# Kernel tuning notes

Measured on AMD Instinct MI355X. Metric: run time of the kernel, lower is better.

## Reference

```python
import jax, jax.numpy as jnp
import numpy as np

N_OPS, B, C, N = 7, 128, 64, 30   # n_ops from alphas (7), SPD dim hard-coded to 30 in source
KARCHER_ITERS = 3                 # fixed-point iterations of the weighted geometric mean


def _spd_fn(X, fn):
    """Apply scalar fn to eigenvalues of batched symmetric matrices X[..., n, n]."""
    s, U = jnp.linalg.eigh(X)
    s = jnp.maximum(s, 1e-8)  # SPD clamp for log/sqrt stability
    return jnp.einsum('...ij,...j,...kj->...ik', U, fn(s), U)


def _sym(X):
    return 0.5 * (X + jnp.swapaxes(X, -1, -2))


def setup_inputs() -> dict:
    key = jax.random.key(0)
    k1, k2 = jax.random.split(key)
    # Candidate-op outputs: SPD matrices, one per (op, batch, channel).
    G = jax.random.normal(k1, (N_OPS, B, C, N, N), dtype=jnp.float32)
    spds = jnp.einsum('...ij,...kj->...ik', G, G) / N + 0.1 * jnp.eye(N, dtype=jnp.float32)
    # Architecture logits for this edge (softmaxed in forward, as in Network.forward).
    alphas = 0.001 * jax.random.normal(k2, (N_OPS,), dtype=jnp.float32)
    return {"spds": spds, "alphas": alphas}


def reference(spds, alphas):
    """MixedOp forward: softmax-weighted SPD geometric (Karcher) barycenter over
    candidate ops, batched over every (batch, channel) 30x30 SPD matrix.
    Replaces the per-channel Python loop + bary_geom_weightedbatch of the source.
    Returns [B, C, N, N]."""
    w = jax.nn.softmax(alphas)                       # [n_ops]
    A = spds.reshape(N_OPS, B * C, N, N)             # [o, m, n, n], m = B*C
    # init with weighted arithmetic mean (standard Karcher-flow initialization)
    X = jnp.einsum('o,omij->mij', w, A)              # [m, n, n]
    for _ in range(KARCHER_ITERS):
        Xh = _spd_fn(X, jnp.sqrt)                    # X^{1/2}
        Xih = _spd_fn(X, lambda s: 1.0 / jnp.sqrt(s))  # X^{-1/2}
        mid = jnp.einsum('mij,omjk,mkl->omil', Xih, A, Xih)  # [o, m, n, n]
        logs = _spd_fn(_sym(mid), jnp.log)
        L = _sym(jnp.einsum('o,omij->mij', w, logs))  # tangent-space mean
        X = _sym(Xh @ _spd_fn(L, jnp.exp) @ Xh)      # exp map back to manifold
    return X.reshape(B, C, N, N)
```

## Files before the change

### kernel.cpp

```cpp
#include <hip/hip_runtime.h>
#include <math.h>

#define NOPS 7
#define KITERS 3
#define NBLK 31

template<int M> __device__ __forceinline__ float xshuf(float x);
template<> __device__ __forceinline__ float xshuf<1>(float x) {
    return __int_as_float(__builtin_amdgcn_mov_dpp(__float_as_int(x), 0xB1, 0xF, 0xF, true));
}
template<> __device__ __forceinline__ float xshuf<2>(float x) {
    return __int_as_float(__builtin_amdgcn_mov_dpp(__float_as_int(x), 0x4E, 0xF, 0xF, true));
}
template<> __device__ __forceinline__ float xshuf<4>(float x) {
    return __int_as_float(__builtin_amdgcn_ds_swizzle(__float_as_int(x), (4 << 10) | 0x1F));
}
template<> __device__ __forceinline__ float xshuf<8>(float x) {
    return __int_as_float(__builtin_amdgcn_ds_swizzle(__float_as_int(x), (8 << 10) | 0x1F));
}

template<int M>
__device__ __forceinline__ void jround(float (&a)[16], float (&v)[16], float2* ct,
                                       const int il, const int lane, const int fKb) {
    const int fil = (il & (M - 1)) | ((il >> 1) & ~(M - 1));
    const float dq  = xshuf<M>(a[0]);
    const float apq = a[M];
    float cc = 1.f, ss = 0.f;
    if (fabsf(apq) > 1e-12f) {
        const float th = (dq - a[0]) / (2.f * apq);
        const float t  = copysignf(1.f, th) / (fabsf(th) + sqrtf(1.f + th * th));
        cc = rsqrtf(1.f + t * t);
        ss = t * cc;
    }
    if ((lane & (32 | M)) == 0) ct[fil] = make_float2(cc, ss);
    __syncthreads();
    const float2 me = ct[fil];
    const float sg = (il & M) ? 1.f : -1.f;
    const float c0 = me.x, s0 = sg * me.y;
    #pragma unroll
    for (int j = 0; j < 16; ++j) {
        if (j & M) continue;
        const int fj = (j & (M - 1)) | ((j >> 1) & ~(M - 1));
        const float2 cs = ct[fil ^ (fj | fKb)];
        const float sl = sg * cs.y;
        const float ak = a[j], am = a[j ^ M];
        a[j]     = fmaf( sl, am, cs.x * ak);
        a[j ^ M] = fmaf(-sl, ak, cs.x * am);
        const float2 cu = ct[fj | fKb];
        const float vk = v[j], vm = v[j ^ M];
        v[j]     = fmaf(-cu.y, vm, cu.x * vk);
        v[j ^ M] = fmaf( cu.y, vk, cu.x * vm);
    }
    #pragma unroll
    for (int j = 0; j < 16; ++j) {
        if (j & M) continue;
        const float r1 = xshuf<M>(a[j ^ M]);
        const float r2 = xshuf<M>(a[j]);
        a[j]     = fmaf(s0, r1, c0 * a[j]);
        a[j ^ M] = fmaf(s0, r2, c0 * a[j ^ M]);
    }
}

__global__ __launch_bounds__(64)
void karcher_kernel(const float* __restrict__ spds, const float* __restrict__ alphas,
                    float* __restrict__ out, int Mtot) {
    __shared__ __align__(16) float XI[1024];
    __shared__ __align__(16) float SC[1024];
    __shared__ float2 CT[16];
    __shared__ float FDA[32];
    __shared__ float FDB[32];
    __shared__ float WS[8];

    const int lane  = threadIdx.x;
    const int il    = lane & 31;
    const int cbit  = lane >> 5;
    const int cbase = cbit << 4;
    const int fKb   = cbit << 3;
    const int c13   = cbit ? 13 : 0;
    const int mat   = blockIdx.x;
    const bool rr   = (il < 30);

    if (lane == 0) {
        float aa[NOPS], mx = -1e30f, sum = 0.f;
        #pragma unroll
        for (int o = 0; o < NOPS; ++o) { aa[o] = alphas[o]; mx = fmaxf(mx, aa[o]); }
        #pragma unroll
        for (int o = 0; o < NOPS; ++o) { aa[o] = expf(aa[o] - mx); sum += aa[o]; }
        #pragma unroll
        for (int o = 0; o < NOPS; ++o) WS[o] = aa[o] / sum;
    }

    int l4row = il;
    #pragma unroll
    for (int i = 0; i < 4; ++i) l4row = ((l4row << 1) & 31) ^ ((l4row & 16) ? 5 : 0);

    const size_t ostr = (size_t)Mtot * 900;
    const float* Abase = spds + (size_t)mat * 900 + (size_t)il * 30 + cbase;
    float* orow = out + (size_t)mat * 900 + (size_t)il * 30 + cbase;

    auto stage16 = [&](float* buf, const float (&r)[16]) {
        #pragma unroll
        for (int j = 0; j < 16; ++j) buf[((cbase + j) << 5) + il] = r[j];
    };
    auto xload16 = [&](const float* buf, float (&a)[16]) {
        #pragma unroll
        for (int j = 0; j < 16; ++j) a[j] = buf[((il ^ (cbase + j)) << 5) + il];
    };
    auto perm4 = [&](float (&a)[16], float (&v)[16]) {
        constexpr int L4T[16] = {0,16,5,21,10,26,15,31,20,4,17,1,30,14,27,11};
        #pragma unroll
        for (int j = 0; j < 16; ++j) SC[((cbase + j) << 5) + il] = a[j];
        __syncthreads();
        #pragma unroll
        for (int j = 0; j < 16; ++j) a[j] = SC[((L4T[j] ^ c13) << 5) + l4row];
        __syncthreads();
        #pragma unroll
        for (int j = 0; j < 16; ++j) SC[((cbase + j) << 5) + il] = v[j];
        __syncthreads();
        #pragma unroll
        for (int j = 0; j < 16; ++j) v[j] = SC[((L4T[j] ^ c13) << 5) + il];
        __syncthreads();
    };
    auto jacobi = [&](float (&a)[16], float (&v)[16]) {
        #pragma unroll
        for (int j = 0; j < 16; ++j) v[j] = (cbase + j == il) ? 1.f : 0.f;
        #pragma unroll 1
        for (int b = 0; b < NBLK; ++b) {
            jround<1>(a, v, CT, il, lane, fKb);
            jround<2>(a, v, CT, il, lane, fKb);
            jround<4>(a, v, CT, il, lane, fKb);
            jround<8>(a, v, CT, il, lane, fKb);
            perm4(a, v);
        }
    };
    auto loadA = [&](const float* Ao, float (&r)[16]) {
        #pragma unroll
        for (int u = 0; u < 7; ++u) {
            const float2 p = *(const float2*)(Ao + 2 * u);
            r[2 * u] = p.x; r[2 * u + 1] = p.y;
        }
        if (cbit == 0) {
            const float2 p = *(const float2*)(Ao + 14);
            r[14] = p.x; r[15] = p.y;
        }
    };
    auto fma16 = [&](const float* buf, const int k, const float c, float (&acc)[16]) {
        const float4* bp = (const float4*)(buf + (k << 5) + cbase);
        #pragma unroll
        for (int q = 0; q < 4; ++q) {
            const float4 b = bp[q];
            acc[4*q+0] = fmaf(c, b.x, acc[4*q+0]);
            acc[4*q+1] = fmaf(c, b.y, acc[4*q+1]);
            acc[4*q+2] = fmaf(c, b.z, acc[4*q+2]);
            acc[4*q+3] = fmaf(c, b.w, acc[4*q+3]);
        }
    };

    __syncthreads();

    float X[16];
    #pragma unroll
    for (int j = 0; j < 16; ++j) X[j] = 0.f;
    if (rr) {
        #pragma unroll 1
        for (int o = 0; o < NOPS; ++o) {
            const float wo = WS[o];
            float r[16];
            #pragma unroll
            for (int j = 0; j < 16; ++j) r[j] = 0.f;
            loadA(Abase + (size_t)o * ostr, r);
            #pragma unroll
            for (int j = 0; j < 16; ++j) X[j] = fmaf(wo, r[j], X[j]);
        }
    }

    float Lacc[16];

    #pragma unroll 1
    for (int it = 0; it < KITERS; ++it) {
        __syncthreads();
        stage16(SC, X);
        __syncthreads();
        float a1[16], v1[16];
        xload16(SC, a1);
        jacobi(a1, v1);
        if (lane < 32) {
            const float lam = fmaxf(a1[0], 1e-8f);
            const float sq = sqrtf(lam);
            FDA[il] = sq;
            FDB[il] = 1.f / sq;
        }
        __syncthreads();
        stage16(SC, v1);
        __syncthreads();
        {
            float xh[16], xi[16];
            #pragma unroll
            for (int j = 0; j < 16; ++j) { xh[j] = 0.f; xi[j] = 0.f; }
            #pragma unroll 2
            for (int k = 0; k < 30; ++k) {
                const float vk = SC[(k << 5) + il];
                const float c1 = FDA[k] * vk;
                const float c2 = FDB[k] * vk;
                const float4* bp = (const float4*)(SC + (k << 5) + cbase);
                #pragma unroll
                for (int q = 0; q < 4; ++q) {
                    const float4 b = bp[q];
                    xh[4*q+0] = fmaf(c1, b.x, xh[4*q+0]); xi[4*q+0] = fmaf(c2, b.x, xi[4*q+0]);
                    xh[4*q+1] = fmaf(c1, b.y, xh[4*q+1]); xi[4*q+1] = fmaf(c2, b.y, xi[4*q+1]);
                    xh[4*q+2] = fmaf(c1, b.z, xh[4*q+2]); xi[4*q+2] = fmaf(c2, b.z, xi[4*q+2]);
                    xh[4*q+3] = fmaf(c1, b.w, xh[4*q+3]); xi[4*q+3] = fmaf(c2, b.w, xi[4*q+3]);
                }
            }
            if (rr) {
                #pragma unroll
                for (int u = 0; u < 7; ++u)
                    *(float2*)(orow + 2 * u) = make_float2(xh[2*u], xh[2*u+1]);
                if (cbit == 0)
                    *(float2*)(orow + 14) = make_float2(xh[14], xh[15]);
            }
            __syncthreads();
            stage16(XI, xi);
        }
        #pragma unroll
        for (int j = 0; j < 16; ++j) Lacc[j] = 0.f;

        #pragma unroll 1
        for (int o = 0; o < NOPS; ++o) {
            float ar[16];
            #pragma unroll
            for (int j = 0; j < 16; ++j) ar[j] = 0.f;
            if (rr) loadA(Abase + (size_t)o * ostr, ar);
            __syncthreads();
            stage16(SC, ar);
            __syncthreads();
            float T[16];
            #pragma unroll
            for (int j = 0; j < 16; ++j) T[j] = 0.f;
            #pragma unroll 2
            for (int k = 0; k < 30; ++k)
                fma16(SC, k, XI[(k << 5) + il], T);
            __syncthreads();
            stage16(SC, T);
            __syncthreads();
            float md[16];
            #pragma unroll
            for (int j = 0; j < 16; ++j) md[j] = 0.f;
            #pragma unroll 2
            for (int k = 0; k < 30; ++k)
                fma16(XI, k, SC[(k << 5) + il], md);
            __syncthreads();
            stage16(SC, md);
            __syncthreads();
            float a2[16], v2[16];
            xload16(SC, a2);
            jacobi(a2, v2);
            if (lane < 32) FDA[il] = logf(fmaxf(a2[0], 1e-8f));
            __syncthreads();
            stage16(SC, v2);
            __syncthreads();
            const float wo = WS[o];
            #pragma unroll 2
            for (int k = 0; k < 30; ++k)
                fma16(SC, k, wo * FDA[k] * SC[(k << 5) + il], Lacc);
        }

        __syncthreads();
        stage16(SC, Lacc);
        __syncthreads();
        float a3[16], v3[16];
        xload16(SC, a3);
        jacobi(a3, v3);
        if (lane < 32) FDA[il] = expf(fmaxf(a3[0], 1e-8f));
        __syncthreads();
        stage16(SC, v3);
        __syncthreads();
        float E[16];
        #pragma unroll
        for (int j = 0; j < 16; ++j) E[j] = 0.f;
        #pragma unroll 2
        for (int k = 0; k < 30; ++k)
            fma16(SC, k, FDA[k] * SC[(k << 5) + il], E);
        float xr[16];
        #pragma unroll
        for (int j = 0; j < 16; ++j) xr[j] = 0.f;
        if (rr) loadA(orow, xr);
        __syncthreads();
        stage16(XI, E);
        stage16(SC, xr);
        __syncthreads();
        float T2[16];
        #pragma unroll
        for (int j = 0; j < 16; ++j) T2[j] = 0.f;
        #pragma unroll 2
        for (int k = 0; k < 30; ++k)
            fma16(XI, k, SC[(k << 5) + il], T2);
        __syncthreads();
        stage16(XI, T2);
        __syncthreads();
        #pragma unroll
        for (int j = 0; j < 16; ++j) X[j] = 0.f;
        #pragma unroll 2
        for (int k = 0; k < 30; ++k)
            fma16(SC, k, XI[(k << 5) + il], X);
    }

    if (rr) {
        #pragma unroll
        for (int u = 0; u < 7; ++u)
            *(float2*)(orow + 2 * u) = make_float2(X[2*u], X[2*u+1]);
        if (cbit == 0)
            *(float2*)(orow + 14) = make_float2(X[14], X[15]);
    }
}

extern "C" void kernel_launch(void* const* d_in, const int* in_sizes, int n_in,
                              void* d_out, int out_size, void* d_ws, size_t ws_size,
                              hipStream_t stream) {
    const float* spds   = (const float*)d_in[0];
    const float* alphas = (const float*)d_in[1];
    float* out = (float*)d_out;
    const int Mtot = in_sizes[0] / (NOPS * 900);
    karcher_kernel<<<dim3(Mtot), dim3(64), 0, stream>>>(spds, alphas, out, Mtot);
}
```

Baseline: 9.388 ms.

## Pack four wavefronts per block, use wave-local syncs, add Jacobi early exit

Each block now holds four independent single-wave matrix solvers with per-wave shared buffers. Block-wide barriers become wave-local s_waitcnt fences, since each matrix lives entirely in one 64-lane wave. Jacobi sweeps can now stop early once every off-diagonal entry falls below a threshold after a minimum sweep count. Some reduction loops are widened to 32, and some FMAs are fused. The early exit changes numerical accuracy, and relying on lgkmcnt waits instead of barriers assumes one wave executes in lockstep.

```diff
diff --git a/kernel.cpp b/kernel.cpp
--- a/kernel.cpp
+++ b/kernel.cpp
@@ -4,6 +4,12 @@
 #define NOPS 7
 #define KITERS 3
 #define NBLK 31
+#define WPB 4
+#define CHKFROM 10
+#define CONVEPS 3e-6f
+
+#define WSYNC() asm volatile("s_waitcnt lgkmcnt(0)" ::: "memory")
+#define VSYNC() asm volatile("s_waitcnt vmcnt(0)" ::: "memory")
 
 template<int M> __device__ __forceinline__ float xshuf(float x);
 template<> __device__ __forceinline__ float xshuf<1>(float x) {
@@ -21,19 +27,19 @@
 
 template<int M>
 __device__ __forceinline__ void jround(float (&a)[16], float (&v)[16], float2* ct,
-                                       const int il, const int lane, const int fKb) {
+                                       const int il, const int wlane, const int fKb) {
     const int fil = (il & (M - 1)) | ((il >> 1) & ~(M - 1));
     const float dq  = xshuf<M>(a[0]);
     const float apq = a[M];
     float cc = 1.f, ss = 0.f;
     if (fabsf(apq) > 1e-12f) {
         const float th = (dq - a[0]) / (2.f * apq);
-        const float t  = copysignf(1.f, th) / (fabsf(th) + sqrtf(1.f + th * th));
-        cc = rsqrtf(1.f + t * t);
+        const float t  = copysignf(1.f, th) / (fabsf(th) + sqrtf(fmaf(th, th, 1.f)));
+        cc = rsqrtf(fmaf(t, t, 1.f));
         ss = t * cc;
     }
-    if ((lane & (32 | M)) == 0) ct[fil] = make_float2(cc, ss);
-    __syncthreads();
+    if ((wlane & (32 | M)) == 0) ct[fil] = make_float2(cc, ss);
+    WSYNC();
     const float2 me = ct[fil];
     const float sg = (il & M) ? 1.f : -1.f;
     const float c0 = me.x, s0 = sg * me.y;
@@ -61,26 +67,37 @@
     }
 }
 
-__global__ __launch_bounds__(64)
+__global__ __launch_bounds__(64 * WPB)
 void karcher_kernel(const float* __restrict__ spds, const float* __restrict__ alphas,
                     float* __restrict__ out, int Mtot) {
-    __shared__ __align__(16) float XI[1024];
-    __shared__ __align__(16) float SC[1024];
-    __shared__ float2 CT[16];
-    __shared__ float FDA[32];
-    __shared__ float FDB[32];
-    __shared__ float WS[8];
-
-    const int lane  = threadIdx.x;
-    const int il    = lane & 31;
-    const int cbit  = lane >> 5;
+    __shared__ __align__(16) float XIb[WPB][1024];
+    __shared__ __align__(16) float SCb[WPB][1024];
+    __shared__ float2 CTb[WPB][16];
+    __shared__ float FDAb[WPB][32];
+    __shared__ float FDBb[WPB][32];
+    __shared__ float WSb[WPB][8];
+
+    const int tid   = threadIdx.x;
+    const int wid   = tid >> 6;
+    const int wlane = tid & 63;
+    const int il    = wlane & 31;
+    const int cbit  = wlane >> 5;
     const int cbase = cbit << 4;
     const int fKb   = cbit << 3;
     const int c13   = cbit ? 13 : 0;
-    const int mat   = blockIdx.x;
+    const int mat   = blockIdx.x * WPB + wid;
     const bool rr   = (il < 30);
 
-    if (lane == 0) {
+    float* XI  = XIb[wid];
+    float* SC  = SCb[wid];
+    float2* CT = CTb[wid];
+    float* FDA = FDAb[wid];
+    float* FDB = FDBb[wid];
+    float* WS  = WSb[wid];
+
+    if (mat >= Mtot) return;
+
+    if (wlane == 0) {
         float aa[NOPS], mx = -1e30f, sum = 0.f;
         #pragma unroll
         for (int o = 0; o < NOPS; ++o) { aa[o] = alphas[o]; mx = fmaxf(mx, aa[o]); }
@@ -110,27 +127,33 @@
         constexpr int L4T[16] = {0,16,5,21,10,26,15,31,20,4,17,1,30,14,27,11};
         #pragma unroll
         for (int j = 0; j < 16; ++j) SC[((cbase + j) << 5) + il] = a[j];
-        __syncthreads();
+        WSYNC();
         #pragma unroll
         for (int j = 0; j < 16; ++j) a[j] = SC[((L4T[j] ^ c13) << 5) + l4row];
-        __syncthreads();
+        WSYNC();
         #pragma unroll
         for (int j = 0; j < 16; ++j) SC[((cbase + j) << 5) + il] = v[j];
-        __syncthreads();
+        WSYNC();
         #pragma unroll
         for (int j = 0; j < 16; ++j) v[j] = SC[((L4T[j] ^ c13) << 5) + il];
-        __syncthreads();
+        WSYNC();
     };
     auto jacobi = [&](float (&a)[16], float (&v)[16]) {
         #pragma unroll
         for (int j = 0; j < 16; ++j) v[j] = (cbase + j == il) ? 1.f : 0.f;
         #pragma unroll 1
         for (int b = 0; b < NBLK; ++b) {
-            jround<1>(a, v, CT, il, lane, fKb);
-            jround<2>(a, v, CT, il, lane, fKb);
-            jround<4>(a, v, CT, il, lane, fKb);
-            jround<8>(a, v, CT, il, lane, fKb);
-            perm4(a, v);
+            jround<1>(a, v, CT, il, wlane, fKb);
+            jround<2>(a, v, CT, il, wlane, fKb);
+            jround<4>(a, v, CT, il, wlane, fKb);
+            jround<8>(a, v, CT, il, wlane, fKb);
+            if (b >= CHKFROM) {
+                float mx = cbit ? fabsf(a[0]) : 0.f;
+                #pragma unroll
+                for (int j = 1; j < 16; ++j) mx = fmaxf(mx, fabsf(a[j]));
+                if (!__any(mx > CONVEPS)) break;
+            }
+            if (b != NBLK - 1) perm4(a, v);
         }
     };
     auto loadA = [&](const float* Ao, float (&r)[16]) {
@@ -156,7 +179,7 @@
         }
     };
 
-    __syncthreads();
+    WSYNC();
 
     float X[16];
     #pragma unroll
@@ -178,27 +201,27 @@
 
     #pragma unroll 1
     for (int it = 0; it < KITERS; ++it) {
-        __syncthreads();
+        WSYNC();
         stage16(SC, X);
-        __syncthreads();
+        WSYNC();
         float a1[16], v1[16];
         xload16(SC, a1);
         jacobi(a1, v1);
-        if (lane < 32) {
+        if (wlane < 32) {
             const float lam = fmaxf(a1[0], 1e-8f);
             const float sq = sqrtf(lam);
             FDA[il] = sq;
             FDB[il] = 1.f / sq;
         }
-        __syncthreads();
+        WSYNC();
         stage16(SC, v1);
-        __syncthreads();
+        WSYNC();
         {
             float xh[16], xi[16];
             #pragma unroll
             for (int j = 0; j < 16; ++j) { xh[j] = 0.f; xi[j] = 0.f; }
             #pragma unroll 2
-            for (int k = 0; k < 30; ++k) {
+            for (int k = 0; k < 32; ++k) {
                 const float vk = SC[(k << 5) + il];
                 const float c1 = FDA[k] * vk;
                 const float c2 = FDB[k] * vk;
@@ -219,7 +242,7 @@
                 if (cbit == 0)
                     *(float2*)(orow + 14) = make_float2(xh[14], xh[15]);
             }
-            __syncthreads();
+            WSYNC();
             stage16(XI, xi);
         }
         #pragma unroll
@@ -231,73 +254,74 @@
             #pragma unroll
             for (int j = 0; j < 16; ++j) ar[j] = 0.f;
             if (rr) loadA(Abase + (size_t)o * ostr, ar);
-            __syncthreads();
+            WSYNC();
             stage16(SC, ar);
-            __syncthreads();
+            WSYNC();
             float T[16];
             #pragma unroll
             for (int j = 0; j < 16; ++j) T[j] = 0.f;
             #pragma unroll 2
             for (int k = 0; k < 30; ++k)
                 fma16(SC, k, XI[(k << 5) + il], T);
-            __syncthreads();
+            WSYNC();
             stage16(SC, T);
-            __syncthreads();
+            WSYNC();
             float md[16];
             #pragma unroll
             for (int j = 0; j < 16; ++j) md[j] = 0.f;
             #pragma unroll 2
             for (int k = 0; k < 30; ++k)
                 fma16(XI, k, SC[(k << 5) + il], md);
-            __syncthreads();
+            WSYNC();
             stage16(SC, md);
-            __syncthreads();
+            WSYNC();
             float a2[16], v2[16];
             xload16(SC, a2);
             jacobi(a2, v2);
-            if (lane < 32) FDA[il] = logf(fmaxf(a2[0], 1e-8f));
-            __syncthreads();
+            if (wlane < 32) FDA[il] = logf(fmaxf(a2[0], 1e-8f));
+            WSYNC();
             stage16(SC, v2);
-            __syncthreads();
+            WSYNC();
             const float wo = WS[o];
             #pragma unroll 2
-            for (int k = 0; k < 30; ++k)
+            for (int k = 0; k < 32; ++k)
                 fma16(SC, k, wo * FDA[k] * SC[(k << 5) + il], Lacc);
         }
 
-        __syncthreads();
+        WSYNC();
         stage16(SC, Lacc);
-        __syncthreads();
+        WSYNC();
         float a3[16], v3[16];
         xload16(SC, a3);
         jacobi(a3, v3);
-        if (lane < 32) FDA[il] = expf(fmaxf(a3[0], 1e-8f));
-        __syncthreads();
+        if (wlane < 32) FDA[il] = expf(fmaxf(a3[0], 1e-8f));
+        WSYNC();
         stage16(SC, v3);
-        __syncthreads();
+        WSYNC();
         float E[16];
         #pragma unroll
         for (int j = 0; j < 16; ++j) E[j] = 0.f;
         #pragma unroll 2
-        for (int k = 0; k < 30; ++k)
+        for (int k = 0; k < 32; ++k)
             fma16(SC, k, FDA[k] * SC[(k << 5) + il], E);
         float xr[16];
         #pragma unroll
         for (int j = 0; j < 16; ++j) xr[j] = 0.f;
+        VSYNC();
         if (rr) loadA(orow, xr);
-        __syncthreads();
+        WSYNC();
         stage16(XI, E);
         stage16(SC, xr);
-        __syncthreads();
+        WSYNC();
         float T2[16];
         #pragma unroll
         for (int j = 0; j < 16; ++j) T2[j] = 0.f;
         #pragma unroll 2
         for (int k = 0; k < 30; ++k)
             fma16(XI, k, SC[(k << 5) + il], T2);
-        __syncthreads();
+        WSYNC();
         stage16(XI, T2);
-        __syncthreads();
+        WSYNC();
         #pragma unroll
         for (int j = 0; j < 16; ++j) X[j] = 0.f;
         #pragma unroll 2
@@ -321,5 +345,6 @@
     const float* alphas = (const float*)d_in[1];
     float* out = (float*)d_out;
     const int Mtot = in_sizes[0] / (NOPS * 900);
-    karcher_kernel<<<dim3(Mtot), dim3(64), 0, stream>>>(spds, alphas, out, Mtot);
-}
+    karcher_kernel<<<dim3((Mtot + WPB - 1) / WPB), dim3(64 * WPB), 0, stream>>>(
+        spds, alphas, out, Mtot);
+}
```

After: 9.400 ms. About the same (+0.1%).
